# Kernel optimization log

Hardware: AMD Instinct MI355X
Metric: run time of the kernel (lower is better)

## Reference

```python
import jax, jax.numpy as jnp
import numpy as np

jax.config.update("jax_enable_x64", True)

DIM = 128          # state dimension
T = 4096           # number of time points
BATCH = 64         # batched initial conditions (columns of x0)
N_UPPER = DIM * (DIM - 1) // 2  # 8128


def setup_inputs() -> dict:
    key = jax.random.key(0)
    k1, k2 = jax.random.split(key)
    return {
        "t": jnp.arange(T, dtype=jnp.float64) * 0.01,               # uniform time grid
        "x0": jax.random.normal(k1, (DIM, BATCH), dtype=jnp.float64),
        "S_upper": jax.random.normal(k2, (N_UPPER,), dtype=jnp.float64) * 0.3,
        "D_raw": jnp.ones((DIM,), dtype=jnp.float64) * 0.1,
    }


def _get_A(S_upper, D_raw):
    # skew-symmetric S from upper-triangular entries, minus positive diagonal D
    iu, ju = np.triu_indices(DIM, k=1)  # static index sets
    S = jnp.zeros((DIM, DIM), dtype=S_upper.dtype).at[iu, ju].set(S_upper)
    S = S - S.T
    return S - jnp.diag(jax.nn.softplus(D_raw))


def reference(t, x0, S_upper, D_raw):
    A = _get_A(S_upper, D_raw)
    dt = t[1] - t[0]
    expAdt = jax.scipy.linalg.expm(A * dt)  # [DIM, DIM]

    def step(x, _):
        x = expAdt @ x  # [DIM, BATCH]
        return x, x

    _, ys = jax.lax.scan(step, x0, None, length=T - 1)  # [T-1, DIM, BATCH]
    return jnp.concatenate([x0[None], ys], axis=0)      # [T, DIM, BATCH]
```

## Files before the change

kernel.cpp:

```cpp
#include <hip/hip_runtime.h>
#include <math.h>

#define DIM 128
#define XA(q)   (((q) - 1) * 16384)
#define GS(s)   ((8 + (s)) * 16384)
#define YF(j)   (14 * 16384 + (j) * 8192)
#define FW      (46 * 16384)
#define FY      (78 * 16384)
#define ALPHA   16.0f

typedef _Float16 f16x8 __attribute__((ext_vector_type(8)));
typedef float    f32x4 __attribute__((ext_vector_type(4)));

__device__ __forceinline__ float4 ld4(const float* p) { return *(const float4*)p; }

__device__ __forceinline__ void stageAT(const float* __restrict__ A, float* AT, int tid)
{
    for (int idx = tid * 4; idx < DIM * DIM; idx += 1024) {
        float4 v = ld4(&A[idx]);
        int d = idx >> 7, k = idx & 127;
        AT[(k + 0) * 132 + d] = v.x;
        AT[(k + 1) * 132 + d] = v.y;
        AT[(k + 2) * 132 + d] = v.z;
        AT[(k + 3) * 132 + d] = v.w;
    }
}

__device__ __forceinline__ void mm_core(const float* AT, const float* Bs,
                                        float (&acc)[4][4], int tid)
{
    int d0 = (tid & 31) * 4, c0 = (tid >> 5) * 4;
    #pragma unroll 4
    for (int k = 0; k < DIM; k++) {
        float4 a4 = ld4(&AT[k * 132 + d0]);
        float4 b4 = ld4(&Bs[k * 36 + c0]);
        float a_[4] = {a4.x, a4.y, a4.z, a4.w};
        float b_[4] = {b4.x, b4.y, b4.z, b4.w};
        #pragma unroll
        for (int i = 0; i < 4; i++)
            #pragma unroll
            for (int j = 0; j < 4; j++) acc[i][j] += a_[i] * b_[j];
    }
}

__global__ __launch_bounds__(256) void k_x2(const float* __restrict__ t,
                                            const float* __restrict__ x0,
                                            const float* __restrict__ S,
                                            const float* __restrict__ D,
                                            float* __restrict__ ws)
{
    __shared__ __align__(16) float AT[DIM * 132];
    __shared__ __align__(16) float Bs[DIM * 36];
    int tid = threadIdx.x, bid = blockIdx.x, cpan = bid * 32;
    float sc = (t[1] - t[0]) * ALPHA;
    for (int e = tid; e < 16384; e += 256) {
        int r = e >> 7, c = e & 127;
        float a;
        if (r == c)      a = -log1pf(expf(D[r]));
        else if (r < c)  a =  S[(r * (2 * DIM - r - 1)) / 2 + (c - r - 1)];
        else             a = -S[(c * (2 * DIM - c - 1)) / 2 + (r - c - 1)];
        a *= sc;
        AT[c * 132 + r] = a;
        if (c >= cpan && c < cpan + 32) Bs[r * 36 + (c - cpan)] = a;
        if (bid == 0) ws[XA(1) + e] = a;
    }
    if (bid == 1) for (int e = tid; e < 8192; e += 256) ws[YF(0) + e] = x0[e];
    if (bid == 2) {
        _Float16* Wf = (_Float16*)(ws + FW);
        for (int ch = tid; ch < 2048; ch += 256) {
            int m = ch >> 4, k0 = (ch & 15) << 3;
            f16x8 hv;
            #pragma unroll
            for (int q = 0; q < 8; q++) hv[q] = (m == k0 + q) ? (_Float16)1.0f : (_Float16)0.0f;
            int lane = (m & 15) | (((k0 >> 3) & 3) << 4);
            size_t off = (((size_t)(m >> 4) * 4 + (k0 >> 5)) * 64 + lane) * 8;
            *(f16x8*)(Wf + off) = hv;
        }
    }
    if (bid == 3) {
        _Float16* Yf = (_Float16*)(ws + FY);
        for (int slot = tid; slot < 1024; slot += 256) {
            int ls = slot & 63, tile = slot >> 6;
            int n = (tile >> 2) * 16 + (ls & 15);
            int k0 = (tile & 3) * 32 + ((ls >> 4) & 3) * 8;
            f16x8 hv;
            #pragma unroll
            for (int q = 0; q < 8; q++) hv[q] = (_Float16)x0[(size_t)(k0 + q) * 64 + n];
            *(f16x8*)(Yf + (size_t)slot * 8) = hv;
        }
    }
    __syncthreads();
    float acc[4][4] = {};
    mm_core(AT, Bs, acc, tid);
    int d0 = (tid & 31) * 4, c0 = (tid >> 5) * 4;
    #pragma unroll
    for (int r = 0; r < 4; r++) {
        float4 st = make_float4(acc[r][0], acc[r][1], acc[r][2], acc[r][3]);
        *(float4*)&ws[XA(2) + (size_t)(d0 + r) * DIM + cpan + c0] = st;
    }
}

struct Jobs { int4 jb[64]; };

__global__ __launch_bounds__(256) void k_lvl(float* __restrict__ ws, Jobs jobs)
{
    __shared__ __align__(16) float AT[DIM * 132];
    __shared__ __align__(16) float Bs[DIM * 36];
    const int4 jb = jobs.jb[blockIdx.x];
    const int cpan  = jb.w & 127;
    const int ncols = (jb.w >> 8) & 255;
    const int fragj = ((jb.w >> 17) & 127) - 1;
    const float* A = ws + jb.x;
    const float* B = ws + jb.y;
    float* C = ws + jb.z;
    const int tid = threadIdx.x;
    stageAT(A, AT, tid);
    for (int s = tid; s < DIM * 8; s += 256) {
        int k = s >> 3, cc4 = (s & 7) * 4;
        *(float4*)&Bs[k * 36 + cc4] = ld4(&B[(size_t)k * ncols + cpan + cc4]);
    }
    __syncthreads();
    float acc[4][4] = {};
    mm_core(AT, Bs, acc, tid);
    int d0 = (tid & 31) * 4, c0 = (tid >> 5) * 4;
    #pragma unroll
    for (int r = 0; r < 4; r++) {
        float4 st = make_float4(acc[r][0], acc[r][1], acc[r][2], acc[r][3]);
        *(float4*)&C[(size_t)(d0 + r) * ncols + cpan + c0] = st;
    }
    if (fragj < 0) return;
    __syncthreads();
    #pragma unroll
    for (int r = 0; r < 4; r++)
        #pragma unroll
        for (int j = 0; j < 4; j++) Bs[(d0 + r) * 36 + c0 + j] = acc[r][j];
    __syncthreads();
    _Float16* Yf = (_Float16*)(ws + FY) + (size_t)fragj * 8192;
    for (int ch = tid; ch < 512; ch += 256) {
        int nloc = ch >> 4, k0 = (ch & 15) * 8;
        f16x8 hv;
        #pragma unroll
        for (int q = 0; q < 8; q++) hv[q] = (_Float16)Bs[(k0 + q) * 36 + nloc];
        int n = cpan + nloc;
        int lane = (n & 15) | (((k0 >> 3) & 3) << 4);
        size_t off = (((size_t)(n >> 4) * 4 + (k0 >> 5)) * 64 + lane) * 8;
        *(f16x8*)(Yf + off) = hv;
    }
}

__global__ __launch_bounds__(256) void k_ps(float* __restrict__ ws)
{
    __shared__ __align__(16) float AT[DIM * 132];
    __shared__ __align__(16) float Bs[DIM * 36];
    int i = blockIdx.x + 1, cpan = blockIdx.y * 32, tid = threadIdx.x;
    float r = (float)i / ALPHA;
    float c[16]; c[0] = 1.0f;
    #pragma unroll
    for (int n = 1; n < 16; n++) c[n] = c[n - 1] * (r / (float)n);
    stageAT(ws + XA(8), AT, tid);
    for (int s = tid; s < DIM * 8; s += 256) {
        int k = s >> 3, cc4 = (s & 7) * 4;
        float4 b = make_float4(0.f, 0.f, 0.f, 0.f);
        #pragma unroll
        for (int q = 1; q < 8; q++) {
            float4 x = ld4(&ws[XA(q) + (size_t)k * DIM + cpan + cc4]);
            b.x += c[8 + q] * x.x; b.y += c[8 + q] * x.y;
            b.z += c[8 + q] * x.z; b.w += c[8 + q] * x.w;
        }
        int col = cpan + cc4;
        if (k >= col && k < col + 4) (&b.x)[k - col] += c[8];
        *(float4*)&Bs[k * 36 + cc4] = b;
    }
    __syncthreads();
    float acc[4][4] = {};
    mm_core(AT, Bs, acc, tid);
    int d0 = (tid & 31) * 4, c0 = (tid >> 5) * 4;
    #pragma unroll
    for (int rr = 0; rr < 4; rr++) {
        int dd = d0 + rr;
        float add[4] = {0.f, 0.f, 0.f, 0.f};
        #pragma unroll
        for (int q = 1; q < 8; q++) {
            float4 x = ld4(&ws[XA(q) + (size_t)dd * DIM + cpan + c0]);
            add[0] += c[q] * x.x; add[1] += c[q] * x.y;
            add[2] += c[q] * x.z; add[3] += c[q] * x.w;
        }
        int col0 = cpan + c0;
        if (dd >= col0 && dd < col0 + 4) add[dd - col0] += 1.0f;
        #pragma unroll
        for (int j = 0; j < 4; j++) acc[rr][j] += add[j];
    }
    if (i == 64) {
        #pragma unroll
        for (int rr = 0; rr < 4; rr++) {
            float4 st = make_float4(acc[rr][0], acc[rr][1], acc[rr][2], acc[rr][3]);
            *(float4*)&ws[GS(0) + (size_t)(d0 + rr) * DIM + cpan + c0] = st;
        }
        return;
    }
    __syncthreads();
    #pragma unroll
    for (int rr = 0; rr < 4; rr++)
        #pragma unroll
        for (int j = 0; j < 4; j++) Bs[(d0 + rr) * 36 + c0 + j] = acc[rr][j];
    __syncthreads();
    _Float16* Wf = (_Float16*)(ws + FW);
    for (int ch = tid; ch < 512; ch += 256) {
        int m = ch >> 2, k0l = (ch & 3) * 8, k0 = cpan + k0l;
        f16x8 hv;
        #pragma unroll
        for (int q = 0; q < 8; q++) hv[q] = (_Float16)Bs[m * 36 + k0l + q];
        int lane = (m & 15) | (((k0 >> 3) & 3) << 4);
        size_t off = (size_t)i * 16384 + (((size_t)(m >> 4) * 4 + (k0 >> 5)) * 64 + lane) * 8;
        *(f16x8*)(Wf + off) = hv;
    }
}

__global__ __launch_bounds__(256) void k_final(const _Float16* __restrict__ Wf,
                                               const _Float16* __restrict__ Yf,
                                               float* __restrict__ out)
{
    int i = blockIdx.x, j = blockIdx.y;
    int tid = threadIdx.x, wave = tid >> 6, lane = tid & 63;
    const _Float16* Ab = Yf + (size_t)j * 8192;
    const _Float16* Bb = Wf + (size_t)i * 16384;
    f32x4 acc[4][2] = {};
    #pragma unroll
    for (int ks = 0; ks < 4; ks++) {
        f16x8 a[4], b[2];
        #pragma unroll
        for (int bt = 0; bt < 4; bt++)
            a[bt] = *(const f16x8*)(Ab + (((size_t)bt * 4 + ks) * 64 + lane) * 8);
        #pragma unroll
        for (int nn = 0; nn < 2; nn++)
            b[nn] = *(const f16x8*)(Bb + (((size_t)(wave * 2 + nn) * 4 + ks) * 64 + lane) * 8);
        #pragma unroll
        for (int bt = 0; bt < 4; bt++)
            #pragma unroll
            for (int nn = 0; nn < 2; nn++)
                acc[bt][nn] = __builtin_amdgcn_mfma_f32_16x16x32_f16(a[bt], b[nn], acc[bt][nn], 0, 0, 0);
    }
    float* slab = out + (size_t)(j * 64 + i) * 8192;
    int nlo = lane & 15, b0 = (lane >> 4) * 4;
    #pragma unroll
    for (int bt = 0; bt < 4; bt++)
        #pragma unroll
        for (int nn = 0; nn < 2; nn++) {
            int n = (wave * 2 + nn) * 16 + nlo;
            __builtin_nontemporal_store(acc[bt][nn],
                (f32x4*)&slab[(size_t)n * 64 + bt * 16 + b0]);
        }
}

static inline void addjob(Jobs& J, int& n, int a, int b, int c,
                          int cpan, int ncols, int fragj)
{
    J.jb[n++] = make_int4(a, b, c, cpan | (ncols << 8) | ((fragj + 1) << 17));
}

static inline void addmm(Jobs& J, int& n, int a, int b, int c, int ncols, int fragj)
{
    for (int p = 0; p < ncols; p += 32) addjob(J, n, a, b, c, p, ncols, fragj);
}

extern "C" void kernel_launch(void* const* d_in, const int* in_sizes, int n_in,
                              void* d_out, int out_size, void* d_ws, size_t ws_size,
                              hipStream_t stream)
{
    const float* t  = (const float*)d_in[0];
    const float* x0 = (const float*)d_in[1];
    const float* S  = (const float*)d_in[2];
    const float* D  = (const float*)d_in[3];
    float* out = (float*)d_out;
    float* ws  = (float*)d_ws;
    _Float16* Wf = (_Float16*)(ws + FW);
    _Float16* Yf = (_Float16*)(ws + FY);

    hipLaunchKernelGGL(k_x2, dim3(4), dim3(256), 0, stream, t, x0, S, D, ws);

    Jobs J; int n;
    n = 0;
    addmm(J, n, XA(2), XA(1), XA(3), 128, -1);
    addmm(J, n, XA(2), XA(2), XA(4), 128, -1);
    hipLaunchKernelGGL(k_lvl, dim3(n), dim3(256), 0, stream, ws, J);
    n = 0;
    for (int q = 1; q <= 4; q++) addmm(J, n, XA(4), XA(q), XA(4 + q), 128, -1);
    hipLaunchKernelGGL(k_lvl, dim3(n), dim3(256), 0, stream, ws, J);

    hipLaunchKernelGGL(k_ps, dim3(64, 4), dim3(256), 0, stream, ws);

    n = 0;
    addmm(J, n, GS(0), GS(0), GS(1), 128, -1);
    addmm(J, n, GS(0), YF(0), YF(1), 64, 1);
    hipLaunchKernelGGL(k_lvl, dim3(n), dim3(256), 0, stream, ws, J);
    n = 0;
    addmm(J, n, GS(1), GS(1), GS(2), 128, -1);
    addmm(J, n, GS(1), YF(0), YF(2), 64, 2);
    addmm(J, n, GS(1), YF(1), YF(3), 64, 3);
    hipLaunchKernelGGL(k_lvl, dim3(n), dim3(256), 0, stream, ws, J);
    n = 0;
    addmm(J, n, GS(2), GS(2), GS(3), 128, -1);
    for (int jj = 0; jj < 4; jj++)
        addmm(J, n, GS(2), YF(jj), YF(4 + jj), 64, 4 + jj);
    hipLaunchKernelGGL(k_lvl, dim3(n), dim3(256), 0, stream, ws, J);
    n = 0;
    addmm(J, n, GS(3), GS(3), GS(4), 128, -1);
    for (int jj = 0; jj < 8; jj++)
        addmm(J, n, GS(3), YF(jj), YF(8 + jj), 64, 8 + jj);
    hipLaunchKernelGGL(k_lvl, dim3(n), dim3(256), 0, stream, ws, J);
    n = 0;
    addmm(J, n, GS(4), GS(4), GS(5), 128, -1);
    for (int jj = 0; jj < 16; jj++)
        addmm(J, n, GS(4), YF(jj), YF(16 + jj), 64, 16 + jj);
    hipLaunchKernelGGL(k_lvl, dim3(n), dim3(256), 0, stream, ws, J);
    n = 0;
    for (int jj = 0; jj < 32; jj++)
        addmm(J, n, GS(5), YF(jj), YF(32 + jj), 64, 32 + jj);
    hipLaunchKernelGGL(k_lvl, dim3(n), dim3(256), 0, stream, ws, J);

    hipLaunchKernelGGL(k_final, dim3(64, 64), dim3(256), 0, stream, Wf, Yf, out);
}
```

Baseline: 214.4 us.

## Fuse last doubling levels into final kernel via split-fp16 G propagation

Drops the last two k_lvl launches that extended the Y fragments from 16 to 64. Instead, the level-3 job writes G^16 as fp16 hi/lo split fragments. k_final recomputes the needed Y fragment by repeatedly applying G^16 (0-3 passes, bouncing through LDS) before the output GEMM. This removes two serialized launches and their global round-trips, but adds redundant MFMA work in every final block and extra fp16 rounding of intermediate states.

```diff
diff --git a/kernel.cpp b/kernel.cpp
--- a/kernel.cpp
+++ b/kernel.cpp
@@ -7,6 +7,8 @@
 #define YF(j)   (14 * 16384 + (j) * 8192)
 #define FW      (46 * 16384)
 #define FY      (78 * 16384)
+#define FGH     (110 * 16384)
+#define FGL     (111 * 16384)
 #define ALPHA   16.0f
 
 typedef _Float16 f16x8 __attribute__((ext_vector_type(8)));
@@ -100,7 +102,7 @@
     }
 }
 
-struct Jobs { int4 jb[64]; };
+struct Jobs { int4 jb[24]; };
 
 __global__ __launch_bounds__(256) void k_lvl(float* __restrict__ ws, Jobs jobs)
 {
@@ -110,6 +112,7 @@
     const int cpan  = jb.w & 127;
     const int ncols = (jb.w >> 8) & 255;
     const int fragj = ((jb.w >> 17) & 127) - 1;
+    const int gmode = (jb.w >> 25) & 1;
     const float* A = ws + jb.x;
     const float* B = ws + jb.y;
     float* C = ws + jb.z;
@@ -128,23 +131,42 @@
         float4 st = make_float4(acc[r][0], acc[r][1], acc[r][2], acc[r][3]);
         *(float4*)&C[(size_t)(d0 + r) * ncols + cpan + c0] = st;
     }
-    if (fragj < 0) return;
+    if (fragj < 0 && !gmode) return;
     __syncthreads();
     #pragma unroll
     for (int r = 0; r < 4; r++)
         #pragma unroll
         for (int j = 0; j < 4; j++) Bs[(d0 + r) * 36 + c0 + j] = acc[r][j];
     __syncthreads();
-    _Float16* Yf = (_Float16*)(ws + FY) + (size_t)fragj * 8192;
-    for (int ch = tid; ch < 512; ch += 256) {
-        int nloc = ch >> 4, k0 = (ch & 15) * 8;
-        f16x8 hv;
-        #pragma unroll
-        for (int q = 0; q < 8; q++) hv[q] = (_Float16)Bs[(k0 + q) * 36 + nloc];
-        int n = cpan + nloc;
-        int lane = (n & 15) | (((k0 >> 3) & 3) << 4);
-        size_t off = (((size_t)(n >> 4) * 4 + (k0 >> 5)) * 64 + lane) * 8;
-        *(f16x8*)(Yf + off) = hv;
+    if (fragj >= 0) {
+        _Float16* Yf = (_Float16*)(ws + FY) + (size_t)fragj * 8192;
+        for (int ch = tid; ch < 512; ch += 256) {
+            int nloc = ch >> 4, k0 = (ch & 15) * 8;
+            f16x8 hv;
+            #pragma unroll
+            for (int q = 0; q < 8; q++) hv[q] = (_Float16)Bs[(k0 + q) * 36 + nloc];
+            int n = cpan + nloc;
+            int lane = (n & 15) | (((k0 >> 3) & 3) << 4);
+            size_t off = (((size_t)(n >> 4) * 4 + (k0 >> 5)) * 64 + lane) * 8;
+            *(f16x8*)(Yf + off) = hv;
+        }
+    } else {
+        _Float16* Gh = (_Float16*)(ws + FGH);
+        _Float16* Gl = (_Float16*)(ws + FGL);
+        for (int ch = tid; ch < 512; ch += 256) {
+            int m = ch >> 2, k0l = (ch & 3) * 8, k0 = cpan + k0l;
+            f16x8 hv, lv;
+            #pragma unroll
+            for (int q = 0; q < 8; q++) {
+                float v = Bs[m * 36 + k0l + q];
+                _Float16 h = (_Float16)v;
+                hv[q] = h; lv[q] = (_Float16)(v - (float)h);
+            }
+            int lane = (m & 15) | (((k0 >> 3) & 3) << 4);
+            size_t off = (((size_t)(m >> 4) * 4 + (k0 >> 5)) * 64 + lane) * 8;
+            *(f16x8*)(Gh + off) = hv;
+            *(f16x8*)(Gl + off) = lv;
+        }
     }
 }
 
@@ -216,51 +238,100 @@
     }
 }
 
-__global__ __launch_bounds__(256) void k_final(const _Float16* __restrict__ Wf,
-                                               const _Float16* __restrict__ Yf,
+__global__ __launch_bounds__(256) void k_final(const float* __restrict__ ws,
                                                float* __restrict__ out)
 {
+    __shared__ _Float16 Yl[64 * 136];
     int i = blockIdx.x, j = blockIdx.y;
     int tid = threadIdx.x, wave = tid >> 6, lane = tid & 63;
-    const _Float16* Ab = Yf + (size_t)j * 8192;
+    const _Float16* Wf = (const _Float16*)(ws + FW);
+    const _Float16* Yf = (const _Float16*)(ws + FY);
+    const _Float16* Gh = (const _Float16*)(ws + FGH);
+    const _Float16* Gl = (const _Float16*)(ws + FGL);
+    const int passes = j >> 4;
+    const int base = j & 15;
+
+    f16x8 ya[4][4];
+    #pragma unroll
+    for (int bt = 0; bt < 4; bt++)
+        #pragma unroll
+        for (int ks = 0; ks < 4; ks++)
+            ya[bt][ks] = *(const f16x8*)(Yf + (size_t)base * 8192 +
+                                         ((size_t)(bt * 4 + ks) * 64 + lane) * 8);
+
+    for (int p = 0; p < passes; p++) {
+        f32x4 pa[4][2] = {};
+        #pragma unroll
+        for (int ks = 0; ks < 4; ks++) {
+            f16x8 gh[2], gl[2];
+            #pragma unroll
+            for (int nn = 0; nn < 2; nn++) {
+                size_t go = (((size_t)(wave * 2 + nn) * 4 + ks) * 64 + lane) * 8;
+                gh[nn] = *(const f16x8*)(Gh + go);
+                gl[nn] = *(const f16x8*)(Gl + go);
+            }
+            #pragma unroll
+            for (int bt = 0; bt < 4; bt++)
+                #pragma unroll
+                for (int nn = 0; nn < 2; nn++) {
+                    pa[bt][nn] = __builtin_amdgcn_mfma_f32_16x16x32_f16(ya[bt][ks], gh[nn], pa[bt][nn], 0, 0, 0);
+                    pa[bt][nn] = __builtin_amdgcn_mfma_f32_16x16x32_f16(ya[bt][ks], gl[nn], pa[bt][nn], 0, 0, 0);
+                }
+        }
+        __syncthreads();
+        #pragma unroll
+        for (int bt = 0; bt < 4; bt++)
+            #pragma unroll
+            for (int nn = 0; nn < 2; nn++) {
+                int kout = (wave * 2 + nn) * 16 + (lane & 15);
+                int b0 = bt * 16 + (lane >> 4) * 4;
+                #pragma unroll
+                for (int q = 0; q < 4; q++)
+                    Yl[(b0 + q) * 136 + kout] = (_Float16)pa[bt][nn][q];
+            }
+        __syncthreads();
+        #pragma unroll
+        for (int bt = 0; bt < 4; bt++)
+            #pragma unroll
+            for (int ks = 0; ks < 4; ks++)
+                ya[bt][ks] = *(const f16x8*)&Yl[(bt * 16 + (lane & 15)) * 136 +
+                                                ks * 32 + ((lane >> 4) & 3) * 8];
+    }
+
     const _Float16* Bb = Wf + (size_t)i * 16384;
     f32x4 acc[4][2] = {};
     #pragma unroll
     for (int ks = 0; ks < 4; ks++) {
-        f16x8 a[4], b[2];
-        #pragma unroll
-        for (int bt = 0; bt < 4; bt++)
-            a[bt] = *(const f16x8*)(Ab + (((size_t)bt * 4 + ks) * 64 + lane) * 8);
-        #pragma unroll
-        for (int nn = 0; nn < 2; nn++)
-            b[nn] = *(const f16x8*)(Bb + (((size_t)(wave * 2 + nn) * 4 + ks) * 64 + lane) * 8);
-        #pragma unroll
-        for (int bt = 0; bt < 4; bt++)
-            #pragma unroll
-            for (int nn = 0; nn < 2; nn++)
-                acc[bt][nn] = __builtin_amdgcn_mfma_f32_16x16x32_f16(a[bt], b[nn], acc[bt][nn], 0, 0, 0);
+        f16x8 b0v = *(const f16x8*)(Bb + (((size_t)(wave * 2 + 0) * 4 + ks) * 64 + lane) * 8);
+        f16x8 b1v = *(const f16x8*)(Bb + (((size_t)(wave * 2 + 1) * 4 + ks) * 64 + lane) * 8);
+        #pragma unroll
+        for (int bt = 0; bt < 4; bt++) {
+            acc[bt][0] = __builtin_amdgcn_mfma_f32_16x16x32_f16(ya[bt][ks], b0v, acc[bt][0], 0, 0, 0);
+            acc[bt][1] = __builtin_amdgcn_mfma_f32_16x16x32_f16(ya[bt][ks], b1v, acc[bt][1], 0, 0, 0);
+        }
     }
     float* slab = out + (size_t)(j * 64 + i) * 8192;
-    int nlo = lane & 15, b0 = (lane >> 4) * 4;
+    int nlo = lane & 15, b0r = (lane >> 4) * 4;
     #pragma unroll
     for (int bt = 0; bt < 4; bt++)
         #pragma unroll
         for (int nn = 0; nn < 2; nn++) {
             int n = (wave * 2 + nn) * 16 + nlo;
             __builtin_nontemporal_store(acc[bt][nn],
-                (f32x4*)&slab[(size_t)n * 64 + bt * 16 + b0]);
+                (f32x4*)&slab[(size_t)n * 64 + bt * 16 + b0r]);
         }
 }
 
 static inline void addjob(Jobs& J, int& n, int a, int b, int c,
-                          int cpan, int ncols, int fragj)
-{
-    J.jb[n++] = make_int4(a, b, c, cpan | (ncols << 8) | ((fragj + 1) << 17));
-}
-
-static inline void addmm(Jobs& J, int& n, int a, int b, int c, int ncols, int fragj)
-{
-    for (int p = 0; p < ncols; p += 32) addjob(J, n, a, b, c, p, ncols, fragj);
+                          int cpan, int ncols, int fragj, int gmode)
+{
+    J.jb[n++] = make_int4(a, b, c, cpan | (ncols << 8) | ((fragj + 1) << 17) | (gmode << 25));
+}
+
+static inline void addmm(Jobs& J, int& n, int a, int b, int c, int ncols,
+                         int fragj, int gmode = 0)
+{
+    for (int p = 0; p < ncols; p += 32) addjob(J, n, a, b, c, p, ncols, fragj, gmode);
 }
 
 extern "C" void kernel_launch(void* const* d_in, const int* in_sizes, int n_in,
@@ -273,8 +344,6 @@
     const float* D  = (const float*)d_in[3];
     float* out = (float*)d_out;
     float* ws  = (float*)d_ws;
-    _Float16* Wf = (_Float16*)(ws + FW);
-    _Float16* Yf = (_Float16*)(ws + FY);
 
     hipLaunchKernelGGL(k_x2, dim3(4), dim3(256), 0, stream, t, x0, S, D, ws);
 
@@ -304,19 +373,10 @@
         addmm(J, n, GS(2), YF(jj), YF(4 + jj), 64, 4 + jj);
     hipLaunchKernelGGL(k_lvl, dim3(n), dim3(256), 0, stream, ws, J);
     n = 0;
-    addmm(J, n, GS(3), GS(3), GS(4), 128, -1);
+    addmm(J, n, GS(3), GS(3), GS(4), 128, -1, 1);
     for (int jj = 0; jj < 8; jj++)
         addmm(J, n, GS(3), YF(jj), YF(8 + jj), 64, 8 + jj);
     hipLaunchKernelGGL(k_lvl, dim3(n), dim3(256), 0, stream, ws, J);
-    n = 0;
-    addmm(J, n, GS(4), GS(4), GS(5), 128, -1);
-    for (int jj = 0; jj < 16; jj++)
-        addmm(J, n, GS(4), YF(jj), YF(16 + jj), 64, 16 + jj);
-    hipLaunchKernelGGL(k_lvl, dim3(n), dim3(256), 0, stream, ws, J);
-    n = 0;
-    for (int jj = 0; jj < 32; jj++)
-        addmm(J, n, GS(5), YF(jj), YF(32 + jj), 64, 32 + jj);
-    hipLaunchKernelGGL(k_lvl, dim3(n), dim3(256), 0, stream, ws, J);
-
-    hipLaunchKernelGGL(k_final, dim3(64, 64), dim3(256), 0, stream, Wf, Yf, out);
-}
+
+    hipLaunchKernelGGL(k_final, dim3(64, 64), dim3(256), 0, stream, ws, out);
+}
```

New measurement: 195.6 us. 8.8% less time.
